# Performance work log

Hardware: AMD Instinct MI355X
Metric: run time of the kernel (lower is better)

Reference implementation:

```python
import jax, jax.numpy as jnp
import numpy as np

B, T, D, H, L = 64, 512, 256, 512, 4


def setup_inputs() -> dict:
    key = jax.random.key(0)
    ks = jax.random.split(key, 1 + 2 * L)
    inp = {"x": jax.random.normal(ks[0], (B, T, D), dtype=jnp.float32)}
    s = 0.05
    for l in range(L):
        in_dim = D if l == 0 else H
        inp[f"W{l}"] = jax.random.normal(ks[1 + 2 * l], (4 * H, in_dim), dtype=jnp.float32) * s
        inp[f"U{l}"] = jax.random.normal(ks[2 + 2 * l], (4 * H, H), dtype=jnp.float32) * s
        inp[f"bw{l}"] = jnp.zeros((4 * H,), dtype=jnp.float32)
        inp[f"bu{l}"] = jnp.zeros((4 * H,), dtype=jnp.float32)
    return inp


def _lstm_forward(x, params):
    # x: [B, T, D]; params: list of (W [4H,in], U [4H,H], bw [4H], bu [4H])
    Bq = x.shape[0]
    h0 = [jnp.zeros((Bq, H), x.dtype) for _ in range(L)]
    c0 = [jnp.zeros((Bq, H), x.dtype) for _ in range(L)]

    def step(carry, x_t):
        hs, cs = carry
        new_h, new_c = [], []
        inp = x_t  # [B, in]
        for (W, U, bw, bu), h_i, c_i in zip(params, hs, cs):
            z = inp @ W.T + bw + h_i @ U.T + bu  # [B, 4H]
            f, i, o, g = jnp.split(z, 4, axis=-1)  # gate order f,i,o,g
            f = jax.nn.sigmoid(f)
            i = jax.nn.sigmoid(i)
            o = jax.nn.sigmoid(o)
            g = jnp.tanh(g)
            c_n = f * c_i + i * g
            h_n = o * jnp.tanh(c_n)
            new_h.append(h_n)
            new_c.append(c_n)
            inp = h_n
        return (new_h, new_c), inp

    (h_f, c_f), out = jax.lax.scan(step, (h0, c0), jnp.swapaxes(x, 0, 1))
    output = jnp.swapaxes(out, 0, 1)  # [B, T, H]
    return output, jnp.stack(h_f), jnp.stack(c_f)


def reference(x, W0, U0, bw0, bu0, W1, U1, bw1, bu1, W2, U2, bw2, bu2, W3, U3, bw3, bu3):
    params = [(W0, U0, bw0, bu0), (W1, U1, bw1, bu1), (W2, U2, bw2, bu2), (W3, U3, bw3, bu3)]
    return _lstm_forward(x, params)
```

## Files before the change

### kernel.cpp

```cpp
#include <hip/hip_runtime.h>

typedef __attribute__((ext_vector_type(8))) short bf16x8;
typedef __attribute__((ext_vector_type(4))) float f32x4;

#define WPL 32
#define NT 256
#define RING 8

__device__ __forceinline__ unsigned short f2bf(float f) {
  unsigned int u = __float_as_uint(f);
  u += 0x7FFFu + ((u >> 16) & 1u);
  return (unsigned short)(u >> 16);
}
__device__ __forceinline__ float sigmoid_fast(float x) {
  return __builtin_amdgcn_rcpf(1.0f + __builtin_amdgcn_exp2f(-1.4426950408889634f * x));
}
__device__ __forceinline__ float tanh_fast(float x) {
  return 1.0f - 2.0f * __builtin_amdgcn_rcpf(
                           1.0f + __builtin_amdgcn_exp2f(2.885390081777927f * x));
}
__device__ __forceinline__ void wait_vm0() {
  asm volatile("s_waitcnt vmcnt(0)" ::: "memory");
  __builtin_amdgcn_sched_barrier(0);
}
#define WAITVM(N)                                         \
  do {                                                    \
    asm volatile("s_waitcnt vmcnt(" #N ")" ::: "memory"); \
    __builtin_amdgcn_sched_barrier(0);                    \
  } while (0)


__global__ void cvt_x_kernel(const float* __restrict__ x,
                             unsigned short* __restrict__ xf) {
  int tid = blockIdx.x * 256 + threadIdx.x;
  int t     = tid >> 11;
  int inner = tid & 2047;
  int lane  = inner & 63;
  int bt    = (inner >> 6) & 3;
  int c     = inner >> 8;
  int b = bt * 16 + (lane & 15);
  int d = c * 32 + (lane >> 4) * 8;
  const float* s = x + ((size_t)b * 512 + t) * 256 + d;
  f32x4 v0 = *(const f32x4*)s;
  f32x4 v1 = *(const f32x4*)(s + 4);
  bf16x8 o;
  o[0] = (short)f2bf(v0[0]); o[1] = (short)f2bf(v0[1]);
  o[2] = (short)f2bf(v0[2]); o[3] = (short)f2bf(v0[3]);
  o[4] = (short)f2bf(v1[0]); o[5] = (short)f2bf(v1[1]);
  o[6] = (short)f2bf(v1[2]); o[7] = (short)f2bf(v1[3]);
  *(bf16x8*)(xf + (size_t)t * 16384 + (size_t)inner * 8) = o;
}

__global__ void cvt_w_kernel(const float* __restrict__ W,
                             const float* __restrict__ U,
                             unsigned short* __restrict__ dst,
                             int C2, int split) {
  int tid = blockIdx.x * 256 + threadIdx.x;
  int lane = tid & 63;
  int c    = (tid >> 6) % C2;
  int rest = tid / (64 * C2);
  int g = rest & 3;
  int w = rest >> 2;
  int row = g * 512 + w * 16 + (lane & 15);
  int k   = c * 32 + (lane >> 4) * 8;
  const float* s = (k < split) ? (W + (size_t)row * split + k)
                               : (U + (size_t)row * 512 + (k - split));
  f32x4 v0 = *(const f32x4*)s;
  f32x4 v1 = *(const f32x4*)(s + 4);
  bf16x8 o;
  o[0] = (short)f2bf(v0[0]); o[1] = (short)f2bf(v0[1]);
  o[2] = (short)f2bf(v0[2]); o[3] = (short)f2bf(v0[3]);
  o[4] = (short)f2bf(v1[0]); o[5] = (short)f2bf(v1[1]);
  o[6] = (short)f2bf(v1[2]); o[7] = (short)f2bf(v1[3]);
  *(bf16x8*)(dst + (size_t)tid * 8) = o;
}

__global__ void bias_kernel(const float* __restrict__ bw,
                            const float* __restrict__ bu,
                            float* __restrict__ dst) {
  int i = blockIdx.x * 256 + threadIdx.x;
  dst[i] = bw[i] + bu[i];
}

__global__ void zero_flags(unsigned int* __restrict__ p) {
  int i = blockIdx.x * 256 + threadIdx.x;
  p[i] = 0u;
}

template <int C1, int C2, bool COH1>
__device__ __forceinline__ void gemm_run(const unsigned short* __restrict__ a1,
                                         const unsigned short* __restrict__ a2,
                                         const char* bg0, const char* bg1,
                                         const char* bg2, const char* bg3,
                                         int voffA, f32x4 acc[4]) {
  constexpr int NP = C2 / 4;
  bf16x8 av[3][4];
  bf16x8 bb[2][4][4];
  const char* bgp[4] = {bg0, bg1, bg2, bg3};

  auto issueA_iter = [&](int cc, int s3, int i) {
    if (cc < C1) {
      int voff = voffA + cc * 4096;
      if constexpr (COH1)
        asm volatile("global_load_dwordx4 %0, %1, %2 sc0 sc1"
                     : "=v"(av[s3][i]) : "v"(voff), "s"(a1));
      else
        asm volatile("global_load_dwordx4 %0, %1, %2"
                     : "=v"(av[s3][i]) : "v"(voff), "s"(a1));
    } else {
      int voff = voffA + (cc - C1) * 4096;
      asm volatile("global_load_dwordx4 %0, %1, %2 sc0 sc1"
                   : "=v"(av[s3][i]) : "v"(voff), "s"(a2));
    }
  };
  auto issueA_phase = [&](int q) {
#pragma unroll
    for (int i = 0; i < 4; ++i) issueA_iter(4 * q + i, q % 3, i);
  };
  auto loadB_phase = [&](int q) {
#pragma unroll
    for (int i = 0; i < 4; ++i)
#pragma unroll
      for (int g = 0; g < 4; ++g)
        bb[q & 1][i][g] = *(const bf16x8*)(bgp[g] + (4 * q + i) * 1024);
  };

#pragma unroll
  for (int q = 0; q < 3; ++q)
    if (q < NP) issueA_phase(q);
  loadB_phase(0);

#pragma unroll
  for (int ph = 0; ph < NP; ++ph) {
    if (ph + 1 < NP) loadB_phase(ph + 1);
    if (ph < NP - 2) {
      WAITVM(8);
    } else if (ph == NP - 2) {
      WAITVM(4);
    } else {
      WAITVM(0);
    }
#pragma unroll
    for (int i = 0; i < 4; ++i)
#pragma unroll
      for (int g = 0; g < 4; ++g)
        acc[g] = __builtin_amdgcn_mfma_f32_16x16x32_bf16(av[ph % 3][i],
                                                         bb[ph & 1][i][g],
                                                         acc[g], 0, 0, 0);
    if (ph + 3 < NP) issueA_phase(ph + 3);
  }
}

__global__ void __launch_bounds__(NT, 1)
lstm_main(const unsigned short* __restrict__ xfrag,
          const unsigned short* __restrict__ wf0,
          const unsigned short* __restrict__ wf1,
          const unsigned short* __restrict__ wf2,
          const unsigned short* __restrict__ wf3,
          const float* __restrict__ bias,
          unsigned short* __restrict__ hbuf,
          unsigned int* __restrict__ flags,
          float* __restrict__ out) {
  extern __shared__ char smem[];

  const int bid   = blockIdx.x;
  const int layer = bid >> 5;
  const int w     = bid & 31;
  const int tid   = threadIdx.x;
  const int lane  = tid & 63;
  const int vm    = tid >> 6;
  const int l15   = lane & 15;
  const int lhi   = lane >> 4;
  const int hcol  = w * 16 + l15;
  const int C2r   = (layer == 0) ? 24 : 32;
  const int HOFF  = 4 * C2r * 64 * 16;

  const unsigned short* wfl =
      (layer == 0) ? wf0 : (layer == 1) ? wf1 : (layer == 2) ? wf2 : wf3;
  const unsigned short* wsl = wfl + (size_t)w * (4 * C2r * 64 * 8);

  for (int i = tid; i < 4 * C2r * 64; i += NT)
    *(f32x4*)(smem + (size_t)i * 16) = *(const f32x4*)(wsl + (size_t)i * 8);
  __syncthreads();

  const char* bg[4];
#pragma unroll
  for (int g = 0; g < 4; ++g) bg[g] = smem + ((size_t)g * C2r * 64 + lane) * 16;

  float bv[4];
#pragma unroll
  for (int g = 0; g < 4; ++g) bv[g] = bias[layer * 2048 + g * 512 + hcol];

  float creg[4];
#pragma unroll
  for (int r = 0; r < 4; ++r) creg[r] = 0.f;

  const int voffA = lane * 16 + vm * 1024;
  const int base_w = (w >> 1) * 2048 + (w & 1) * 256;

  const unsigned short* hbase_prev =
      (layer == 0) ? nullptr : (hbuf + (size_t)(layer - 1) * RING * 32768);
  const unsigned short* hbase_self = hbuf + (size_t)layer * RING * 32768;

  const int sb_bt = tid >> 5;
  const int sb_q  = (tid >> 4) & 1;
  const int sb_bl = tid & 15;

  for (int t = 0; t < 512; ++t) {
    if (vm == 0) {
      const unsigned int* fp = flags;
      unsigned int need = 0;
      if (lane < 32) {
        if (layer > 0) { fp = flags + ((layer - 1) * 32 + lane) * 16; need = (unsigned)(t + 1); }
      } else {
        if (t > 0) { fp = flags + (layer * 32 + (lane - 32)) * 16; need = (unsigned)t; }
      }
      while (true) {
        unsigned int v = need ? __hip_atomic_load(fp, __ATOMIC_RELAXED,
                                                  __HIP_MEMORY_SCOPE_AGENT) : 0u;
        if (__ballot(need && v < need) == 0) break;
        __builtin_amdgcn_s_sleep(1);
      }
    } else if (vm == 1) {
      const unsigned int* fp = flags;
      unsigned int need = 0;
      if (lane < 32 && layer < 3 && t >= RING) {
        fp = flags + ((layer + 1) * 32 + lane) * 16;
        need = (unsigned)(t - RING + 1);
      }
      while (true) {
        unsigned int v = need ? __hip_atomic_load(fp, __ATOMIC_RELAXED,
                                                  __HIP_MEMORY_SCOPE_AGENT) : 0u;
        if (__ballot(need && v < need) == 0) break;
        __builtin_amdgcn_s_sleep(1);
      }
    }
    __syncthreads();

    const unsigned short* a1 =
        (layer == 0) ? (xfrag + (size_t)t * 16384)
                     : (hbase_prev + (size_t)(t & (RING - 1)) * 32768);
    const unsigned short* a2 =
        hbase_self + (size_t)((t - 1) & (RING - 1)) * 32768;

    f32x4 acc[4];
    const f32x4 z4 = {0.f, 0.f, 0.f, 0.f};
#pragma unroll
    for (int g = 0; g < 4; ++g) acc[g] = z4;

    if (t == 0) {
      if (layer == 0)
        gemm_run<8, 8, false>(a1, a1, bg[0], bg[1], bg[2], bg[3], voffA, acc);
      else
        gemm_run<16, 16, true>(a1, a1, bg[0], bg[1], bg[2], bg[3], voffA, acc);
    } else {
      if (layer == 0)
        gemm_run<8, 24, false>(a1, a2, bg[0], bg[1], bg[2], bg[3], voffA, acc);
      else
        gemm_run<16, 32, true>(a1, a2, bg[0], bg[1], bg[2], bg[3], voffA, acc);
    }

    float hreg[4], cnreg[4];
#pragma unroll
    for (int r = 0; r < 4; ++r) {
      float fg = sigmoid_fast(acc[0][r] + bv[0]);
      float ig = sigmoid_fast(acc[1][r] + bv[1]);
      float og = sigmoid_fast(acc[2][r] + bv[2]);
      float gg = tanh_fast(acc[3][r] + bv[3]);
      float cn = fg * creg[r] + ig * gg;
      creg[r] = cn;
      cnreg[r] = cn;
      float h = og * tanh_fast(cn);
      hreg[r] = h;
      *(unsigned short*)(smem + HOFF + (vm * 16 + lhi * 4 + r) * 32 + l15 * 2) =
          f2bf(h);
    }
    __syncthreads();

    if (tid < 128) {
      f32x4 hv = *(const f32x4*)(smem + HOFF + (sb_bt * 16 + sb_bl) * 32 + sb_q * 16);
      unsigned short* dst = hbuf +
          ((size_t)layer * RING + (t & (RING - 1))) * 32768 +
          base_w + sb_bt * 512 + sb_q * 128 + sb_bl * 8;
      asm volatile("global_store_dwordx4 %0, %1, off sc0 sc1"
                   :: "v"(dst), "v"(hv) : "memory");
      wait_vm0();
    }
    __syncthreads();
    if (tid == 0)
      __hip_atomic_store(flags + (layer * 32 + w) * 16, (unsigned)(t + 1),
                         __ATOMIC_RELAXED, __HIP_MEMORY_SCOPE_AGENT);

    if (layer == 3) {
#pragma unroll
      for (int r = 0; r < 4; ++r) {
        int bidx = vm * 16 + lhi * 4 + r;
        out[(size_t)bidx * 262144 + (size_t)t * 512 + hcol] = hreg[r];
      }
    }
    if (t == 511) {
#pragma unroll
      for (int r = 0; r < 4; ++r) {
        int bidx = vm * 16 + lhi * 4 + r;
        out[16777216 + ((size_t)layer * 64 + bidx) * 512 + hcol] = hreg[r];
        out[16777216 + 131072 + ((size_t)layer * 64 + bidx) * 512 + hcol] = cnreg[r];
      }
    }
  }
}

extern "C" void kernel_launch(void* const* d_in, const int* in_sizes, int n_in,
                              void* d_out, int out_size, void* d_ws, size_t ws_size,
                              hipStream_t stream) {
  const float* x = (const float*)d_in[0];
  const float *W[4], *U[4], *bw[4], *bu[4];
  for (int l = 0; l < 4; ++l) {
    W[l]  = (const float*)d_in[1 + 4 * l];
    U[l]  = (const float*)d_in[2 + 4 * l];
    bw[l] = (const float*)d_in[3 + 4 * l];
    bu[l] = (const float*)d_in[4 + 4 * l];
  }

  char* ws = (char*)d_ws;
  unsigned short* xfrag = (unsigned short*)(ws + 0);
  unsigned short* wfr0  = (unsigned short*)(ws + 16777216);
  unsigned short* wfr1  = (unsigned short*)(ws + 19922944);
  unsigned short* wfr2  = (unsigned short*)(ws + 24117248);
  unsigned short* wfr3  = (unsigned short*)(ws + 28311552);
  float*          biasp = (float*)(ws + 32505856);
  unsigned short* hbuf  = (unsigned short*)(ws + 32538624);
  unsigned int*   flags = (unsigned int*)(ws + 34635776);
  float* out = (float*)d_out;

  cvt_x_kernel<<<4096, 256, 0, stream>>>(x, xfrag);
  cvt_w_kernel<<<768, 256, 0, stream>>>(W[0], U[0], wfr0, 24, 256);
  cvt_w_kernel<<<1024, 256, 0, stream>>>(W[1], U[1], wfr1, 32, 512);
  cvt_w_kernel<<<1024, 256, 0, stream>>>(W[2], U[2], wfr2, 32, 512);
  cvt_w_kernel<<<1024, 256, 0, stream>>>(W[3], U[3], wfr3, 32, 512);
  bias_kernel<<<8, 256, 0, stream>>>(bw[0], bu[0], biasp + 0 * 2048);
  bias_kernel<<<8, 256, 0, stream>>>(bw[1], bu[1], biasp + 1 * 2048);
  bias_kernel<<<8, 256, 0, stream>>>(bw[2], bu[2], biasp + 2 * 2048);
  bias_kernel<<<8, 256, 0, stream>>>(bw[3], bu[3], biasp + 3 * 2048);
  zero_flags<<<8, 256, 0, stream>>>(flags);

  hipFuncSetAttribute((const void*)lstm_main,
                      hipFuncAttributeMaxDynamicSharedMemorySize, 135168);
  lstm_main<<<dim3(4 * WPL), dim3(NT), 135168, stream>>>(
      xfrag, wfr0, wfr1, wfr2, wfr3, biasp, hbuf, flags, out);
}
```

Measured before the change: 1.886 ms.

## Split LSTM step GEMM to overlap input projection with recurrent-flag wait

Each timestep's gate GEMM is split into two parts. The input-projection part (x or previous layer's h) runs first, and only then does the block wait for its own layer's flags before running the recurrent U part. This hides the intra-layer synchronization latency behind the W part of the GEMM, at the cost of an extra __syncthreads per step and a separate load pipeline prologue for each part. Flag loads and stores also switch from HIP atomics to inline-asm sc0 sc1 loads and stores.

```diff
diff --git a/kernel.cpp b/kernel.cpp
--- a/kernel.cpp
+++ b/kernel.cpp
@@ -28,6 +28,28 @@
     asm volatile("s_waitcnt vmcnt(" #N ")" ::: "memory"); \
     __builtin_amdgcn_sched_barrier(0);                    \
   } while (0)
+
+template <int MODE>
+__device__ __forceinline__ void ldA(bf16x8& d, int voff, const unsigned short* base) {
+  if constexpr (MODE == 0)
+    asm volatile("global_load_dwordx4 %0, %1, %2"
+                 : "=v"(d) : "v"(voff), "s"(base));
+  else
+    asm volatile("global_load_dwordx4 %0, %1, %2 sc0 sc1"
+                 : "=v"(d) : "v"(voff), "s"(base));
+}
+__device__ __forceinline__ unsigned ld_flag(const unsigned* p) {
+  unsigned v;
+  asm volatile("global_load_dword %0, %1, off sc0 sc1\n\ts_waitcnt vmcnt(0)"
+               : "=v"(v) : "v"(p) : "memory");
+  return v;
+}
+__device__ __forceinline__ void st16_coh(void* p, f32x4 v) {
+  asm volatile("global_store_dwordx4 %0, %1, off sc0 sc1" :: "v"(p), "v"(v) : "memory");
+}
+__device__ __forceinline__ void st4_coh(void* p, unsigned v) {
+  asm volatile("global_store_dword %0, %1, off sc0 sc1" :: "v"(p), "v"(v) : "memory");
+}
 
 
 __global__ void cvt_x_kernel(const float* __restrict__ x,
@@ -87,35 +109,20 @@
   p[i] = 0u;
 }
 
-template <int C1, int C2, bool COH1>
-__device__ __forceinline__ void gemm_run(const unsigned short* __restrict__ a1,
-                                         const unsigned short* __restrict__ a2,
-                                         const char* bg0, const char* bg1,
-                                         const char* bg2, const char* bg3,
-                                         int voffA, f32x4 acc[4]) {
-  constexpr int NP = C2 / 4;
+template <int NC, int MODE>
+__device__ __forceinline__ void gemm_part(const unsigned short* __restrict__ a,
+                                          const char* bg0, const char* bg1,
+                                          const char* bg2, const char* bg3,
+                                          int voffA, f32x4 acc[4]) {
+  constexpr int NP = NC / 4;
   bf16x8 av[3][4];
   bf16x8 bb[2][4][4];
   const char* bgp[4] = {bg0, bg1, bg2, bg3};
 
-  auto issueA_iter = [&](int cc, int s3, int i) {
-    if (cc < C1) {
-      int voff = voffA + cc * 4096;
-      if constexpr (COH1)
-        asm volatile("global_load_dwordx4 %0, %1, %2 sc0 sc1"
-                     : "=v"(av[s3][i]) : "v"(voff), "s"(a1));
-      else
-        asm volatile("global_load_dwordx4 %0, %1, %2"
-                     : "=v"(av[s3][i]) : "v"(voff), "s"(a1));
-    } else {
-      int voff = voffA + (cc - C1) * 4096;
-      asm volatile("global_load_dwordx4 %0, %1, %2 sc0 sc1"
-                   : "=v"(av[s3][i]) : "v"(voff), "s"(a2));
-    }
-  };
   auto issueA_phase = [&](int q) {
 #pragma unroll
-    for (int i = 0; i < 4; ++i) issueA_iter(4 * q + i, q % 3, i);
+    for (int i = 0; i < 4; ++i)
+      ldA<MODE>(av[q % 3][i], voffA + (4 * q + i) * 4096, a);
   };
   auto loadB_phase = [&](int q) {
 #pragma unroll
@@ -173,6 +180,7 @@
   const int lhi   = lane >> 4;
   const int hcol  = w * 16 + l15;
   const int C2r   = (layer == 0) ? 24 : 32;
+  const int C1w   = (layer == 0) ? 8 : 16;
   const int HOFF  = 4 * C2r * 64 * 16;
 
   const unsigned short* wfl =
@@ -183,9 +191,13 @@
     *(f32x4*)(smem + (size_t)i * 16) = *(const f32x4*)(wsl + (size_t)i * 8);
   __syncthreads();
 
-  const char* bg[4];
-#pragma unroll
-  for (int g = 0; g < 4; ++g) bg[g] = smem + ((size_t)g * C2r * 64 + lane) * 16;
+  const char* bgW[4];
+  const char* bgU[4];
+#pragma unroll
+  for (int g = 0; g < 4; ++g) {
+    bgW[g] = smem + ((size_t)g * C2r * 64 + lane) * 16;
+    bgU[g] = bgW[g] + (size_t)C1w * 1024;
+  }
 
   float bv[4];
 #pragma unroll
@@ -198,66 +210,74 @@
   const int voffA = lane * 16 + vm * 1024;
   const int base_w = (w >> 1) * 2048 + (w & 1) * 256;
 
-  const unsigned short* hbase_prev =
+  const unsigned short* hprev =
       (layer == 0) ? nullptr : (hbuf + (size_t)(layer - 1) * RING * 32768);
-  const unsigned short* hbase_self = hbuf + (size_t)layer * RING * 32768;
+  const unsigned short* hself = hbuf + (size_t)layer * RING * 32768;
 
   const int sb_bt = tid >> 5;
   const int sb_q  = (tid >> 4) & 1;
   const int sb_bl = tid & 15;
+  const int slot_off = base_w + sb_bt * 512 + sb_q * 128 + sb_bl * 8;
 
   for (int t = 0; t < 512; ++t) {
     if (vm == 0) {
-      const unsigned int* fp = flags;
-      unsigned int need = 0;
-      if (lane < 32) {
-        if (layer > 0) { fp = flags + ((layer - 1) * 32 + lane) * 16; need = (unsigned)(t + 1); }
-      } else {
-        if (t > 0) { fp = flags + (layer * 32 + (lane - 32)) * 16; need = (unsigned)t; }
+      const unsigned* fp = flags;
+      unsigned need = 0;
+      if (lane < 32 && layer > 0) {
+        fp = flags + ((layer - 1) * 32 + lane) * 16;
+        need = (unsigned)(t + 1);
       }
       while (true) {
-        unsigned int v = need ? __hip_atomic_load(fp, __ATOMIC_RELAXED,
-                                                  __HIP_MEMORY_SCOPE_AGENT) : 0u;
+        unsigned v = need ? ld_flag(fp) : 0u;
         if (__ballot(need && v < need) == 0) break;
         __builtin_amdgcn_s_sleep(1);
       }
     } else if (vm == 1) {
-      const unsigned int* fp = flags;
-      unsigned int need = 0;
+      const unsigned* fp = flags;
+      unsigned need = 0;
       if (lane < 32 && layer < 3 && t >= RING) {
         fp = flags + ((layer + 1) * 32 + lane) * 16;
         need = (unsigned)(t - RING + 1);
       }
       while (true) {
-        unsigned int v = need ? __hip_atomic_load(fp, __ATOMIC_RELAXED,
-                                                  __HIP_MEMORY_SCOPE_AGENT) : 0u;
+        unsigned v = need ? ld_flag(fp) : 0u;
         if (__ballot(need && v < need) == 0) break;
         __builtin_amdgcn_s_sleep(1);
       }
     }
     __syncthreads();
-
-    const unsigned short* a1 =
-        (layer == 0) ? (xfrag + (size_t)t * 16384)
-                     : (hbase_prev + (size_t)(t & (RING - 1)) * 32768);
-    const unsigned short* a2 =
-        hbase_self + (size_t)((t - 1) & (RING - 1)) * 32768;
+    wait_vm0();
 
     f32x4 acc[4];
     const f32x4 z4 = {0.f, 0.f, 0.f, 0.f};
 #pragma unroll
     for (int g = 0; g < 4; ++g) acc[g] = z4;
 
-    if (t == 0) {
-      if (layer == 0)
-        gemm_run<8, 8, false>(a1, a1, bg[0], bg[1], bg[2], bg[3], voffA, acc);
-      else
-        gemm_run<16, 16, true>(a1, a1, bg[0], bg[1], bg[2], bg[3], voffA, acc);
-    } else {
-      if (layer == 0)
-        gemm_run<8, 24, false>(a1, a2, bg[0], bg[1], bg[2], bg[3], voffA, acc);
-      else
-        gemm_run<16, 32, true>(a1, a2, bg[0], bg[1], bg[2], bg[3], voffA, acc);
+    if (layer == 0)
+      gemm_part<8, 0>(xfrag + (size_t)t * 16384,
+                      bgW[0], bgW[1], bgW[2], bgW[3], voffA, acc);
+    else
+      gemm_part<16, 2>(hprev + (size_t)(t & (RING - 1)) * 32768,
+                       bgW[0], bgW[1], bgW[2], bgW[3], voffA, acc);
+
+    if (t > 0) {
+      if (vm == 0) {
+        const unsigned* fp = flags;
+        unsigned need = 0;
+        if (lane < 32) {
+          fp = flags + (layer * 32 + lane) * 16;
+          need = (unsigned)t;
+        }
+        while (true) {
+          unsigned v = need ? ld_flag(fp) : 0u;
+          if (__ballot(need && v < need) == 0) break;
+          __builtin_amdgcn_s_sleep(1);
+        }
+      }
+      __syncthreads();
+
+      gemm_part<16, 2>(hself + (size_t)((t - 1) & (RING - 1)) * 32768,
+                       bgU[0], bgU[1], bgU[2], bgU[3], voffA, acc);
     }
 
     float hreg[4], cnreg[4];
@@ -280,16 +300,13 @@
     if (tid < 128) {
       f32x4 hv = *(const f32x4*)(smem + HOFF + (sb_bt * 16 + sb_bl) * 32 + sb_q * 16);
       unsigned short* dst = hbuf +
-          ((size_t)layer * RING + (t & (RING - 1))) * 32768 +
-          base_w + sb_bt * 512 + sb_q * 128 + sb_bl * 8;
-      asm volatile("global_store_dwordx4 %0, %1, off sc0 sc1"
-                   :: "v"(dst), "v"(hv) : "memory");
+          ((size_t)layer * RING + (t & (RING - 1))) * 32768 + slot_off;
+      st16_coh(dst, hv);
       wait_vm0();
     }
     __syncthreads();
     if (tid == 0)
-      __hip_atomic_store(flags + (layer * 32 + w) * 16, (unsigned)(t + 1),
-                         __ATOMIC_RELAXED, __HIP_MEMORY_SCOPE_AGENT);
+      st4_coh(flags + (layer * 32 + w) * 16, (unsigned)(t + 1));
 
     if (layer == 3) {
 #pragma unroll
```

Measured after the change: 1.876 ms, median of 2. About the same (-0.6%).
